# Optimization experiments

Measured on AMD Instinct MI355X. Metric: run time of the kernel, lower is better.

The kernel has to match this reference:

```python
import jax, jax.numpy as jnp
import numpy as np

B, L, D = 2, 1024, 1024
H = 16
NL = 2
DFF = 4 * D
EPS = 1e-5
W_SCALE = 0.02


def rmsnorm(x, w):
    # x * rsqrt(mean(x^2, -1) + eps) * w   (computed in fp32 as in the torch code)
    xf = x.astype(jnp.float32)
    n = xf * jax.lax.rsqrt(jnp.mean(xf * xf, axis=-1, keepdims=True) + EPS)
    return n.astype(x.dtype) * w


def setup_inputs() -> dict:
    key = jax.random.key(0)
    ks = jax.random.split(key, 10)
    x = jax.random.normal(ks[0], (B, L, D), dtype=jnp.float32)
    # torch nn.Linear weight layout: [out_features, in_features]; y = x @ W.T + b
    qw = jax.random.normal(ks[1], (NL, D, D), dtype=jnp.float32) * W_SCALE
    kw = jax.random.normal(ks[2], (NL, D, D), dtype=jnp.float32) * W_SCALE
    vw = jax.random.normal(ks[3], (NL, D, D), dtype=jnp.float32) * W_SCALE
    ow = jax.random.normal(ks[4], (NL, D, D), dtype=jnp.float32) * W_SCALE
    pn_w = jnp.ones((NL, D), dtype=jnp.float32)
    ln_w = jnp.ones((NL, D), dtype=jnp.float32)
    fc_w = jax.random.normal(ks[5], (NL, DFF, D), dtype=jnp.float32) * W_SCALE
    fc2_w = jax.random.normal(ks[6], (NL, D, DFF), dtype=jnp.float32) * W_SCALE
    fc2_b = jnp.zeros((NL, D), dtype=jnp.float32)
    return {"x": x, "qw": qw, "kw": kw, "vw": vw, "ow": ow,
            "pn_w": pn_w, "ln_w": ln_w, "fc_w": fc_w, "fc2_w": fc2_w, "fc2_b": fc2_b}


def reference(x, qw, kw, vw, ow, pn_w, ln_w, fc_w, fc2_w, fc2_b):
    d = D // H
    for i in range(NL):
        # --- LinearAttention block (dropout=0 -> identity) ---
        h = rmsnorm(x, pn_w[i])                                   # [B,L,D]
        Q = (h @ qw[i].T).reshape(B, L, H, d)
        K = (h @ kw[i].T).reshape(B, L, H, d)
        V = (h @ vw[i].T).reshape(B, L, H, d)
        # outer-product state per position, cumulated over L (causal linear attn)
        W = jnp.einsum('blhd,blhe->blhde', K, V)                  # [B,L,H,d,d]
        W = jnp.cumsum(W, axis=1)
        a = jnp.einsum('blhd,blhde->blhe', Q, W).reshape(B, L, D)
        x = x + a @ ow[i].T
        # --- MLP block ---
        m = rmsnorm(x, ln_w[i])
        f = jax.nn.gelu(m @ fc_w[i].T, approximate=False)         # torch nn.GELU default = exact
        x = x + f @ fc2_w[i].T + fc2_b[i]
    return x
```

## Files before the change

kernel.cpp:

```cpp
#include <hip/hip_runtime.h>

#define BB 2
#define LL 1024
#define DD 1024
#define HH 16
#define HD 64
#define DFFN 4096
#define MM (BB*LL)
#define QS 3072

using u16 = unsigned short;
typedef __bf16 bf16x8 __attribute__((ext_vector_type(8)));
typedef float f32x4 __attribute__((ext_vector_type(4)));

__device__ __forceinline__ float b2f(u16 u) {
  union { unsigned int i; float f; } v; v.i = ((unsigned int)u) << 16; return v.f;
}
__device__ __forceinline__ u16 f2b(float f) {
  union { float f; unsigned int i; } v; v.f = f;
  unsigned int x = v.i;
  return (u16)((x + 0x7fffu + ((x >> 16) & 1u)) >> 16);
}
__device__ __forceinline__ float gelu_exact(float x) {
  return 0.5f * x * (1.0f + erff(x * 0.70710678118654752f));
}
__device__ __forceinline__ void gl2lds16(const void* g, void* l) {
  __builtin_amdgcn_global_load_lds((const __attribute__((address_space(1))) void*)g,
                                   (__attribute__((address_space(3))) void*)l, 16, 0, 0);
}

template<int N>
__device__ __forceinline__ void s_wait_vm() {
  if constexpr (N == 0)       asm volatile("s_waitcnt vmcnt(0)" ::: "memory");
  else if constexpr (N == 3)  asm volatile("s_waitcnt vmcnt(3)" ::: "memory");
  else if constexpr (N == 6)  asm volatile("s_waitcnt vmcnt(6)" ::: "memory");
  __builtin_amdgcn_sched_barrier(0);
}

__device__ __forceinline__ void xcd_remap(int& bx, int& by, int& bz) {
  const int gx = gridDim.x, gy = gridDim.y;
  const int nb = gx * gy * gridDim.z;
  int b = blockIdx.x + gx * (blockIdx.y + gy * blockIdx.z);
  if ((nb & 127) == 0) {
    const int xcd = b & 7, seq = b >> 3;
    b = (((seq >> 4) << 3) + xcd) * 16 + (seq & 15);
  }
  bx = b % gx; const int rest = b / gx;
  by = rest % gy; bz = rest / gy;
}

__global__ __launch_bounds__(256) void castw_kernel(const float* __restrict__ in,
                                                    u16* __restrict__ out, int n8) {
  int i = blockIdx.x * 256 + threadIdx.x;
  if (i >= n8) return;
  const float4 a = reinterpret_cast<const float4*>(in)[2 * i];
  const float4 b = reinterpret_cast<const float4*>(in)[2 * i + 1];
  uint4 o;
  o.x = (unsigned)f2b(a.x) | ((unsigned)f2b(a.y) << 16);
  o.y = (unsigned)f2b(a.z) | ((unsigned)f2b(a.w) << 16);
  o.z = (unsigned)f2b(b.x) | ((unsigned)f2b(b.y) << 16);
  o.w = (unsigned)f2b(b.z) | ((unsigned)f2b(b.w) << 16);
  reinterpret_cast<uint4*>(out)[i] = o;
}
__global__ __launch_bounds__(256) void castw3_kernel(const float* __restrict__ s0,
                                                     const float* __restrict__ s1,
                                                     const float* __restrict__ s2,
                                                     u16* __restrict__ out, int n8) {
  int i = blockIdx.x * 256 + threadIdx.x;
  if (i >= n8) return;
  const float* in = (blockIdx.y == 0) ? s0 : (blockIdx.y == 1) ? s1 : s2;
  u16* dst = out + (size_t)blockIdx.y * n8 * 8;
  const float4 a = reinterpret_cast<const float4*>(in)[2 * i];
  const float4 b = reinterpret_cast<const float4*>(in)[2 * i + 1];
  uint4 o;
  o.x = (unsigned)f2b(a.x) | ((unsigned)f2b(a.y) << 16);
  o.y = (unsigned)f2b(a.z) | ((unsigned)f2b(a.w) << 16);
  o.z = (unsigned)f2b(b.x) | ((unsigned)f2b(b.y) << 16);
  o.w = (unsigned)f2b(b.z) | ((unsigned)f2b(b.w) << 16);
  reinterpret_cast<uint4*>(dst)[i] = o;
}

__global__ __launch_bounds__(256) void init_out_kernel(float* __restrict__ out,
                                                       const float* __restrict__ resid,
                                                       const float* __restrict__ bias) {
  const int i = blockIdx.x * 256 + threadIdx.x;
  float4 v = reinterpret_cast<const float4*>(resid)[i];
  if (bias != nullptr) {
    const float4 bv = *reinterpret_cast<const float4*>(bias + ((i * 4) & (DD - 1)));
    v.x += bv.x; v.y += bv.y; v.z += bv.z; v.w += bv.w;
  }
  reinterpret_cast<float4*>(out)[i] = v;
}

__global__ __launch_bounds__(256) void rmsnorm_kernel(const float* __restrict__ x,
                                                      const float* __restrict__ w,
                                                      u16* __restrict__ out) {
  const int row = blockIdx.x, t = threadIdx.x;
  const float4 v = reinterpret_cast<const float4*>(x + (size_t)row * DD)[t];
  float ss = v.x*v.x + v.y*v.y + v.z*v.z + v.w*v.w;
  #pragma unroll
  for (int o = 32; o > 0; o >>= 1) ss += __shfl_down(ss, o);
  __shared__ float red[4];
  if ((t & 63) == 0) red[t >> 6] = ss;
  __syncthreads();
  const float inv = rsqrtf((red[0] + red[1] + red[2] + red[3]) * (1.0f / DD) + 1e-5f);
  const float4 wv = reinterpret_cast<const float4*>(w)[t];
  ushort4 o;
  o.x = f2b(v.x * inv * wv.x);
  o.y = f2b(v.y * inv * wv.y);
  o.z = f2b(v.z * inv * wv.z);
  o.w = f2b(v.w * inv * wv.w);
  reinterpret_cast<ushort4*>(out + (size_t)row * DD)[t] = o;
}

template<int ROWS, int NT>
__device__ __forceinline__ void dma32(const u16* __restrict__ g, int r0, int K, int kt,
                                      int t, u16* lds) {
  #pragma unroll
  for (int i = 0; i < ROWS * 4 / NT; i++) {
    const int c = i * NT + t;
    const int row = (c & 7) | ((c >> 5) << 3);
    const int kc = (c >> 3) & 3;
    gl2lds16(g + (size_t)(r0 + row) * K + kt + kc * 8, &lds[c * 8]);
  }
}
__device__ __forceinline__ const bf16x8* lds_frag(const u16* base, int r, int fq) {
  const int p = (r & 7) | (fq << 3) | ((r >> 3) << 5);
  return reinterpret_cast<const bf16x8*>(&base[p * 8]);
}

#define MFMA_BF16 __builtin_amdgcn_mfma_f32_16x16x32_bf16

template<int BM, int BN>
__device__ __forceinline__ void gemm_pipe(const u16* __restrict__ A,
                                          const u16* __restrict__ Wb,
                                          int K, int k0, int nt, int m0, int n0,
                                          u16* As, u16* Bs, int t,
                                          int wm, int wn, int fr, int fq,
                                          f32x4 acc[4][4]) {
  constexpr int NT = (BM / 64) * (BN / 64) * 64;
  #pragma unroll
  for (int s = 0; s < 3; ++s) {
    dma32<BM, NT>(A, m0, K, k0 + s * 32, t, As + s * BM * 32);
    dma32<BN, NT>(Wb, n0, K, k0 + s * 32, t, Bs + s * BN * 32);
  }
  s_wait_vm<6>();
  __builtin_amdgcn_s_barrier();
  int pb = 0;
  for (int tt = 0; tt < nt; ++tt) {
    const u16* Asb = As + pb * BM * 32;
    const u16* Bsb = Bs + pb * BN * 32;
    const int p3 = (pb + 3) & 3;
    const bool st = (tt + 3 < nt);
    bf16x8 a0 = *lds_frag(Asb, wm + 0 * 16 + fr, fq);
    bf16x8 a1 = *lds_frag(Asb, wm + 1 * 16 + fr, fq);
    bf16x8 b0 = *lds_frag(Bsb, wn + 0 * 16 + fr, fq);
    bf16x8 b1 = *lds_frag(Bsb, wn + 1 * 16 + fr, fq);
    bf16x8 b2 = *lds_frag(Bsb, wn + 2 * 16 + fr, fq);
    bf16x8 b3 = *lds_frag(Bsb, wn + 3 * 16 + fr, fq);
    if (st) dma32<BM, NT>(A, m0, K, k0 + (tt + 3) * 32, t, As + p3 * BM * 32);
    __builtin_amdgcn_sched_barrier(0);
    __builtin_amdgcn_s_barrier();
    asm volatile("s_waitcnt lgkmcnt(0)" ::: "memory");
    __builtin_amdgcn_sched_barrier(0);
    __builtin_amdgcn_s_setprio(1);
    acc[0][0] = MFMA_BF16(a0, b0, acc[0][0], 0, 0, 0);
    acc[0][1] = MFMA_BF16(a0, b1, acc[0][1], 0, 0, 0);
    acc[0][2] = MFMA_BF16(a0, b2, acc[0][2], 0, 0, 0);
    acc[0][3] = MFMA_BF16(a0, b3, acc[0][3], 0, 0, 0);
    acc[1][0] = MFMA_BF16(a1, b0, acc[1][0], 0, 0, 0);
    acc[1][1] = MFMA_BF16(a1, b1, acc[1][1], 0, 0, 0);
    acc[1][2] = MFMA_BF16(a1, b2, acc[1][2], 0, 0, 0);
    acc[1][3] = MFMA_BF16(a1, b3, acc[1][3], 0, 0, 0);
    __builtin_amdgcn_s_setprio(0);
    __builtin_amdgcn_sched_barrier(0);
    __builtin_amdgcn_s_barrier();
    bf16x8 a2 = *lds_frag(Asb, wm + 2 * 16 + fr, fq);
    bf16x8 a3 = *lds_frag(Asb, wm + 3 * 16 + fr, fq);
    if (st) dma32<BN, NT>(Wb, n0, K, k0 + (tt + 3) * 32, t, Bs + p3 * BN * 32);
    __builtin_amdgcn_sched_barrier(0);
    __builtin_amdgcn_s_barrier();
    asm volatile("s_waitcnt lgkmcnt(0)" ::: "memory");
    __builtin_amdgcn_sched_barrier(0);
    __builtin_amdgcn_s_setprio(1);
    acc[2][0] = MFMA_BF16(a2, b0, acc[2][0], 0, 0, 0);
    acc[2][1] = MFMA_BF16(a2, b1, acc[2][1], 0, 0, 0);
    acc[2][2] = MFMA_BF16(a2, b2, acc[2][2], 0, 0, 0);
    acc[2][3] = MFMA_BF16(a2, b3, acc[2][3], 0, 0, 0);
    acc[3][0] = MFMA_BF16(a3, b0, acc[3][0], 0, 0, 0);
    acc[3][1] = MFMA_BF16(a3, b1, acc[3][1], 0, 0, 0);
    acc[3][2] = MFMA_BF16(a3, b2, acc[3][2], 0, 0, 0);
    acc[3][3] = MFMA_BF16(a3, b3, acc[3][3], 0, 0, 0);
    __builtin_amdgcn_s_setprio(0);
    __builtin_amdgcn_sched_barrier(0);
    if (tt + 1 < nt) {
      const int rem = nt - 2 - tt;
      if (rem >= 2)      s_wait_vm<6>();
      else if (rem == 1) s_wait_vm<3>();
      else               s_wait_vm<0>();
      __builtin_amdgcn_s_barrier();
    }
    pb = (pb + 1) & 3;
  }
}

template<int BM, int BN, int ACT>
__global__ __launch_bounds__((BM/64)*(BN/64)*64)
void mfma_gemm(const u16* __restrict__ A, const u16* __restrict__ Wb,
               u16* __restrict__ Cb, int N, int K) {
  constexpr int WCOLS = BN / 64;
  __shared__ u16 As[4 * BM * 32];
  __shared__ u16 Bs[4 * BN * 32];
  int bx, by, bz;
  xcd_remap(bx, by, bz);
  const int t = threadIdx.x;
  const int lane = t & 63, w = t >> 6;
  const int wm = (w / WCOLS) * 64, wn = (w % WCOLS) * 64;
  const int m0 = by * BM, n0 = bx * BN;
  const int fr = lane & 15, fq = lane >> 4;

  f32x4 acc[4][4] = {};
  gemm_pipe<BM, BN>(A, Wb, K, 0, K / 32, m0, n0, As, Bs, t, wm, wn, fr, fq, acc);

  #pragma unroll
  for (int i = 0; i < 4; i++)
    #pragma unroll
    for (int j = 0; j < 4; j++)
      #pragma unroll
      for (int r = 0; r < 4; r++) {
        const int row = m0 + wm + i * 16 + fq * 4 + r;
        const int col = n0 + wn + j * 16 + fr;
        float val = acc[i][j][r];
        if (ACT == 1) val = gelu_exact(val);
        Cb[(size_t)row * N + col] = f2b(val);
      }
}

template<int BM, int BN, int SPLIT>
__global__ __launch_bounds__((BM/64)*(BN/64)*64)
void mfma_gemm_sk(const u16* __restrict__ A, const u16* __restrict__ Wb,
                  float* __restrict__ Co, int N, int K) {
  constexpr int WCOLS = BN / 64;
  __shared__ u16 As[4 * BM * 32];
  __shared__ u16 Bs[4 * BN * 32];
  int bx, by, bz;
  xcd_remap(bx, by, bz);
  const int t = threadIdx.x;
  const int lane = t & 63, w = t >> 6;
  const int wm = (w / WCOLS) * 64, wn = (w % WCOLS) * 64;
  const int m0 = by * BM, n0 = bx * BN;
  const int fr = lane & 15, fq = lane >> 4;
  const int Kc = K / SPLIT, k0 = bz * Kc;

  f32x4 acc[4][4] = {};
  gemm_pipe<BM, BN>(A, Wb, K, k0, Kc / 32, m0, n0, As, Bs, t, wm, wn, fr, fq, acc);

  #pragma unroll
  for (int i = 0; i < 4; i++)
    #pragma unroll
    for (int j = 0; j < 4; j++)
      #pragma unroll
      for (int r = 0; r < 4; r++) {
        const int row = m0 + wm + i * 16 + fq * 4 + r;
        const int col = n0 + wn + j * 16 + fr;
        unsafeAtomicAdd(&Co[(size_t)row * N + col], acc[i][j][r]);
      }
}

__global__ __launch_bounds__(256) void kv_trans(const u16* __restrict__ QKV,
                                                u16* __restrict__ Kt, u16* __restrict__ Vt) {
  __shared__ u16 T[64][72];
  const int tile = blockIdx.x;
  const int h2 = blockIdx.y;
  const int b = blockIdx.z;
  const int h = h2 & 15, which = h2 >> 4;
  const int t = threadIdx.x;
  const int pos = t >> 2, d0 = (t & 3) * 16;
  const u16* src = QKV + ((size_t)(b * LL) + tile * 64 + pos) * QS + 1024 + which * 1024 + h * HD + d0;
  union { uint4 u[2]; u16 s[16]; } pk;
  pk.u[0] = reinterpret_cast<const uint4*>(src)[0];
  pk.u[1] = reinterpret_cast<const uint4*>(src)[1];
  #pragma unroll
  for (int j = 0; j < 16; j++) T[d0 + j][pos] = pk.s[j];
  __syncthreads();
  const int d = t >> 2, p0 = (t & 3) * 16;
  u16* dst = (which ? Vt : Kt) + ((size_t)(b * HH + h) * HD + d) * LL + tile * 64 + p0;
  union { uint4 u[2]; u16 s[16]; } ok;
  #pragma unroll
  for (int j = 0; j < 16; j++) ok.s[j] = T[d][p0 + j];
  reinterpret_cast<uint4*>(dst)[0] = ok.u[0];
  reinterpret_cast<uint4*>(dst)[1] = ok.u[1];
}

__global__ __launch_bounds__(256) void attn_phase1(const u16* __restrict__ QKV,
                                                   const u16* __restrict__ Kt,
                                                   const u16* __restrict__ Vt,
                                                   u16* __restrict__ Oa,
                                                   u16* __restrict__ Slt) {
  __shared__ u16 Ss[4][16][64];
  const int tile = blockIdx.x, h = blockIdx.y, b = blockIdx.z;
  const int t = threadIdx.x, lane = t & 63, w = t >> 6;
  const int fr = lane & 15, fq = lane >> 4;
  const size_t tok0 = (size_t)(b * LL + tile * 64);
  const size_t bh = (size_t)(b * HH + h);
  const u16* Qb  = QKV + tok0 * QS + h * HD;
  const u16* Kb  = Qb + 1024;
  const u16* Ktb = Kt + bh * (HD * LL) + tile * 64;
  const u16* Vtb = Vt + bh * (HD * LL) + tile * 64;

  bf16x8 aq[2], bk[4][2];
  #pragma unroll
  for (int kh = 0; kh < 2; kh++)
    aq[kh] = *reinterpret_cast<const bf16x8*>(Qb + (size_t)(16*w + fr) * QS + kh*32 + fq*8);
  #pragma unroll
  for (int n4 = 0; n4 < 4; n4++)
    #pragma unroll
    for (int kh = 0; kh < 2; kh++)
      bk[n4][kh] = *reinterpret_cast<const bf16x8*>(Kb + (size_t)(16*n4 + fr) * QS + kh*32 + fq*8);
  f32x4 sacc[4] = {};
  #pragma unroll
  for (int n4 = 0; n4 < 4; n4++) {
    sacc[n4] = MFMA_BF16(aq[0], bk[n4][0], sacc[n4], 0, 0, 0);
    sacc[n4] = MFMA_BF16(aq[1], bk[n4][1], sacc[n4], 0, 0, 0);
  }
  #pragma unroll
  for (int n4 = 0; n4 < 4; n4++)
    #pragma unroll
    for (int r = 0; r < 4; r++) {
      const bool keep = (16*w + 4*fq + r) >= (16*n4 + fr);
      Ss[w][4*fq + r][16*n4 + fr] = keep ? f2b(sacc[n4][r]) : (u16)0;
    }
  __syncthreads();

  bf16x8 va[2], kt[4][2];
  #pragma unroll
  for (int kh = 0; kh < 2; kh++)
    va[kh] = *reinterpret_cast<const bf16x8*>(Vtb + (size_t)(16*w + fr) * LL + kh*32 + fq*8);
  #pragma unroll
  for (int n4 = 0; n4 < 4; n4++)
    #pragma unroll
    for (int kh = 0; kh < 2; kh++)
      kt[n4][kh] = *reinterpret_cast<const bf16x8*>(Ktb + (size_t)(16*n4 + fr) * LL + kh*32 + fq*8);
  f32x4 lacc[4] = {};
  #pragma unroll
  for (int n4 = 0; n4 < 4; n4++) {
    lacc[n4] = MFMA_BF16(va[0], kt[n4][0], lacc[n4], 0, 0, 0);
    lacc[n4] = MFMA_BF16(va[1], kt[n4][1], lacc[n4], 0, 0, 0);
  }
  u16* So = Slt + (bh * 16 + tile) * 4096;
  #pragma unroll
  for (int n4 = 0; n4 < 4; n4++)
    #pragma unroll
    for (int r = 0; r < 4; r++)
      So[(size_t)(16*w + 4*fq + r) * 64 + 16*n4 + fr] = f2b(lacc[n4][r]);

  bf16x8 sa[2], vb[4][2];
  #pragma unroll
  for (int kh = 0; kh < 2; kh++)
    sa[kh] = *reinterpret_cast<const bf16x8*>(&Ss[w][fr][kh*32 + fq*8]);
  #pragma unroll
  for (int n4 = 0; n4 < 4; n4++)
    #pragma unroll
    for (int kh = 0; kh < 2; kh++)
      vb[n4][kh] = *reinterpret_cast<const bf16x8*>(Vtb + (size_t)(16*n4 + fr) * LL + kh*32 + fq*8);
  f32x4 oacc[4] = {};
  #pragma unroll
  for (int n4 = 0; n4 < 4; n4++) {
    oacc[n4] = MFMA_BF16(sa[0], vb[n4][0], oacc[n4], 0, 0, 0);
    oacc[n4] = MFMA_BF16(sa[1], vb[n4][1], oacc[n4], 0, 0, 0);
  }
  u16* Ob = Oa + (tok0 + 16*w) * DD + h * HD;
  #pragma unroll
  for (int n4 = 0; n4 < 4; n4++)
    #pragma unroll
    for (int r = 0; r < 4; r++)
      Ob[(size_t)(4*fq + r) * DD + 16*n4 + fr] = f2b(oacc[n4][r]);
}

__global__ __launch_bounds__(256) void attn_phase2(const u16* __restrict__ Slt,
                                                   u16* __restrict__ Wc) {
  const int rg = blockIdx.x, h = blockIdx.y, b = blockIdx.z;
  const size_t base = ((size_t)((b * HH + h) * 16)) * 4096 + rg * 512 + threadIdx.x * 2;
  float r0 = 0.f, r1 = 0.f;
  for (int tl = 0; tl < 16; tl++) {
    const size_t p = base + (size_t)tl * 4096;
    const unsigned d = *reinterpret_cast<const unsigned*>(Slt + p);
    *reinterpret_cast<unsigned*>(Wc + p) = (unsigned)f2b(r0) | ((unsigned)f2b(r1) << 16);
    r0 += b2f((u16)(d & 0xffff));
    r1 += b2f((u16)(d >> 16));
  }
}

__global__ __launch_bounds__(256) void attn_phase3(const u16* __restrict__ QKV,
                                                   const u16* __restrict__ Wc,
                                                   u16* __restrict__ Oa) {
  const int tile = blockIdx.x, h = blockIdx.y, b = blockIdx.z;
  const int t = threadIdx.x, lane = t & 63, w = t >> 6;
  const int fr = lane & 15, fq = lane >> 4;
  const size_t tok0 = (size_t)(b * LL + tile * 64);
  const size_t bh = (size_t)(b * HH + h);
  const u16* Qb = QKV + tok0 * QS + h * HD;
  const u16* Wb = Wc + (bh * 16 + tile) * 4096;

  bf16x8 aq[2], wb[4][2];
  #pragma unroll
  for (int kh = 0; kh < 2; kh++)
    aq[kh] = *reinterpret_cast<const bf16x8*>(Qb + (size_t)(16*w + fr) * QS + kh*32 + fq*8);
  #pragma unroll
  for (int n4 = 0; n4 < 4; n4++)
    #pragma unroll
    for (int kh = 0; kh < 2; kh++)
      wb[n4][kh] = *reinterpret_cast<const bf16x8*>(Wb + (size_t)(16*n4 + fr) * 64 + kh*32 + fq*8);
  f32x4 oacc[4] = {};
  #pragma unroll
  for (int n4 = 0; n4 < 4; n4++) {
    oacc[n4] = MFMA_BF16(aq[0], wb[n4][0], oacc[n4], 0, 0, 0);
    oacc[n4] = MFMA_BF16(aq[1], wb[n4][1], oacc[n4], 0, 0, 0);
  }
  u16* Ob = Oa + (tok0 + 16*w) * DD + h * HD;
  #pragma unroll
  for (int n4 = 0; n4 < 4; n4++)
    #pragma unroll
    for (int r = 0; r < 4; r++) {
      const size_t idx = (size_t)(4*fq + r) * DD + 16*n4 + fr;
      Ob[idx] = f2b(b2f(Ob[idx]) + oacc[n4][r]);
    }
}

extern "C" void kernel_launch(void* const* d_in, const int* in_sizes, int n_in,
                              void* d_out, int out_size, void* d_ws, size_t ws_size,
                              hipStream_t stream) {
  const float* x_in = (const float*)d_in[0];
  const float* qw   = (const float*)d_in[1];
  const float* kw   = (const float*)d_in[2];
  const float* vw   = (const float*)d_in[3];
  const float* ow   = (const float*)d_in[4];
  const float* pn   = (const float*)d_in[5];
  const float* ln   = (const float*)d_in[6];
  const float* fcw  = (const float*)d_in[7];
  const float* fc2w = (const float*)d_in[8];
  const float* fc2b = (const float*)d_in[9];

  char* ws = (char*)d_ws;
  u16* wbuf = (u16*)ws;
  u16* slt  = (u16*)ws;
  u16* wcum = (u16*)(ws + (size_t)(4 << 20));
  u16* h    = (u16*)(ws + (size_t)(8 << 20));
  u16* qkv  = (u16*)(ws + (size_t)(12 << 20));
  u16* f    = (u16*)(ws + (size_t)(12 << 20));
  u16* vt   = (u16*)(ws + (size_t)(24 << 20));
  u16* kt   = (u16*)(ws + (size_t)(28 << 20));
  float* xf = (float*)d_out;

  const int n8D = DD * DD / 8;
  const int n8F = DFFN * DD / 8;
  const int gInit = MM * DD / 4 / 256;

  for (int i = 0; i < 2; i++) {
    const float* qwi  = qw   + (size_t)i * DD * DD;
    const float* kwi  = kw   + (size_t)i * DD * DD;
    const float* vwi  = vw   + (size_t)i * DD * DD;
    const float* owi  = ow   + (size_t)i * DD * DD;
    const float* fcwi = fcw  + (size_t)i * DFFN * DD;
    const float* f2wi = fc2w + (size_t)i * DD * DFFN;
    const float* src  = (i == 0) ? x_in : xf;

    rmsnorm_kernel<<<MM, 256, 0, stream>>>(src, pn + i * DD, h);
    castw3_kernel<<<dim3(n8D / 256, 3), 256, 0, stream>>>(qwi, kwi, vwi, wbuf, n8D);
    mfma_gemm<256, 128, 0><<<dim3(QS / 128, MM / 256), 512, 0, stream>>>(
        h, wbuf, qkv, QS, DD);
    kv_trans<<<dim3(16, 32, BB), 256, 0, stream>>>(qkv, kt, vt);
    attn_phase1<<<dim3(16, HH, BB), 256, 0, stream>>>(qkv, kt, vt, h, slt);
    attn_phase2<<<dim3(8, HH, BB), 256, 0, stream>>>(slt, wcum);
    attn_phase3<<<dim3(16, HH, BB), 256, 0, stream>>>(qkv, wcum, h);
    castw_kernel<<<n8D / 256, 256, 0, stream>>>(owi, wbuf, n8D);
    init_out_kernel<<<gInit, 256, 0, stream>>>(xf, src, nullptr);
    mfma_gemm_sk<256, 128, 4><<<dim3(DD / 128, MM / 256, 4), 512, 0, stream>>>(
        h, wbuf, xf, DD, DD);
    rmsnorm_kernel<<<MM, 256, 0, stream>>>(xf, ln + i * DD, h);
    castw_kernel<<<n8F / 256, 256, 0, stream>>>(fcwi, wbuf, n8F);
    mfma_gemm<256, 128, 1><<<dim3(DFFN / 128, MM / 256), 512, 0, stream>>>(
        h, wbuf, f, DFFN, DD);
    castw_kernel<<<n8F / 256, 256, 0, stream>>>(f2wi, wbuf, n8F);
    float* co = (i == 1) ? (float*)d_out : xf;
    init_out_kernel<<<gInit, 256, 0, stream>>>(co, xf, fc2b + i * DD);
    mfma_gemm_sk<256, 128, 4><<<dim3(DD / 128, MM / 256, 4), 512, 0, stream>>>(
        f, wbuf, co, DD, DFFN);
  }
}
```

Measured before the change: 581.5 us.

## Replace atomic split-K output GEMMs with fused residual epilogue and partial buffers

Drops the init_out kernels and the atomic split-K accumulation. The O-projection now runs as a single-pass 128x64 tile GEMM whose epilogue adds the residual directly. FC2 uses a 2-way split where slice 0 writes residual+bias+acc and slice 1 writes fp32 partials, which a separate reduce kernel adds back. The pipeline wait counts are generalized for smaller tiles. This removes atomics and an extra full pass over the output, at the cost of smaller tiles with fewer threads, a partial buffer round-trip, and a new reduce launch.

```diff
diff --git a/kernel.cpp b/kernel.cpp
--- a/kernel.cpp
+++ b/kernel.cpp
@@ -34,6 +34,7 @@
   if constexpr (N == 0)       asm volatile("s_waitcnt vmcnt(0)" ::: "memory");
   else if constexpr (N == 3)  asm volatile("s_waitcnt vmcnt(3)" ::: "memory");
   else if constexpr (N == 6)  asm volatile("s_waitcnt vmcnt(6)" ::: "memory");
+  else if constexpr (N == 12) asm volatile("s_waitcnt vmcnt(12)" ::: "memory");
   __builtin_amdgcn_sched_barrier(0);
 }
 
@@ -80,18 +81,6 @@
   reinterpret_cast<uint4*>(dst)[i] = o;
 }
 
-__global__ __launch_bounds__(256) void init_out_kernel(float* __restrict__ out,
-                                                       const float* __restrict__ resid,
-                                                       const float* __restrict__ bias) {
-  const int i = blockIdx.x * 256 + threadIdx.x;
-  float4 v = reinterpret_cast<const float4*>(resid)[i];
-  if (bias != nullptr) {
-    const float4 bv = *reinterpret_cast<const float4*>(bias + ((i * 4) & (DD - 1)));
-    v.x += bv.x; v.y += bv.y; v.z += bv.z; v.w += bv.w;
-  }
-  reinterpret_cast<float4*>(out)[i] = v;
-}
-
 __global__ __launch_bounds__(256) void rmsnorm_kernel(const float* __restrict__ x,
                                                       const float* __restrict__ w,
                                                       u16* __restrict__ out) {
@@ -113,6 +102,18 @@
   reinterpret_cast<ushort4*>(out + (size_t)row * DD)[t] = o;
 }
 
+__global__ __launch_bounds__(256) void reduce_add_kernel(float* __restrict__ co,
+                                                         const float* __restrict__ P0,
+                                                         const float* __restrict__ P1) {
+  const int i = blockIdx.x * 256 + threadIdx.x;
+  constexpr int HALF = (MM / 2) * DD / 4;
+  const float4 p = (i < HALF) ? reinterpret_cast<const float4*>(P0)[i]
+                              : reinterpret_cast<const float4*>(P1)[i - HALF];
+  float4 v = reinterpret_cast<float4*>(co)[i];
+  v.x += p.x; v.y += p.y; v.z += p.z; v.w += p.w;
+  reinterpret_cast<float4*>(co)[i] = v;
+}
+
 template<int ROWS, int NT>
 __device__ __forceinline__ void dma32(const u16* __restrict__ g, int r0, int K, int kt,
                                       int t, u16* lds) {
@@ -139,12 +140,13 @@
                                           int wm, int wn, int fr, int fq,
                                           f32x4 acc[4][4]) {
   constexpr int NT = (BM / 64) * (BN / 64) * 64;
+  constexpr int LT = (BM + BN) * 4 / NT;
   #pragma unroll
   for (int s = 0; s < 3; ++s) {
     dma32<BM, NT>(A, m0, K, k0 + s * 32, t, As + s * BM * 32);
     dma32<BN, NT>(Wb, n0, K, k0 + s * 32, t, Bs + s * BN * 32);
   }
-  s_wait_vm<6>();
+  s_wait_vm<2 * LT>();
   __builtin_amdgcn_s_barrier();
   int pb = 0;
   for (int tt = 0; tt < nt; ++tt) {
@@ -195,8 +197,8 @@
     __builtin_amdgcn_sched_barrier(0);
     if (tt + 1 < nt) {
       const int rem = nt - 2 - tt;
-      if (rem >= 2)      s_wait_vm<6>();
-      else if (rem == 1) s_wait_vm<3>();
+      if (rem >= 2)      s_wait_vm<2 * LT>();
+      else if (rem == 1) s_wait_vm<LT>();
       else               s_wait_vm<0>();
       __builtin_amdgcn_s_barrier();
     }
@@ -236,10 +238,12 @@
       }
 }
 
-template<int BM, int BN, int SPLIT>
+template<int BM, int BN>
 __global__ __launch_bounds__((BM/64)*(BN/64)*64)
-void mfma_gemm_sk(const u16* __restrict__ A, const u16* __restrict__ Wb,
-                  float* __restrict__ Co, int N, int K) {
+void mfma_gemm_fo(const u16* __restrict__ A, const u16* __restrict__ Wb,
+                  const float* __restrict__ resid, const float* __restrict__ bias,
+                  float* __restrict__ Co, float* __restrict__ P0, float* __restrict__ P1,
+                  int N, int K, int Kc) {
   constexpr int WCOLS = BN / 64;
   __shared__ u16 As[4 * BM * 32];
   __shared__ u16 Bs[4 * BN * 32];
@@ -250,21 +254,39 @@
   const int wm = (w / WCOLS) * 64, wn = (w % WCOLS) * 64;
   const int m0 = by * BM, n0 = bx * BN;
   const int fr = lane & 15, fq = lane >> 4;
-  const int Kc = K / SPLIT, k0 = bz * Kc;
+  const int k0 = bz * Kc;
 
   f32x4 acc[4][4] = {};
   gemm_pipe<BM, BN>(A, Wb, K, k0, Kc / 32, m0, n0, As, Bs, t, wm, wn, fr, fq, acc);
 
-  #pragma unroll
-  for (int i = 0; i < 4; i++)
-    #pragma unroll
-    for (int j = 0; j < 4; j++)
+  if (bz == 0) {
+    #pragma unroll
+    for (int j = 0; j < 4; j++) {
+      const int col = n0 + wn + j * 16 + fr;
+      const float bj = (bias != nullptr) ? bias[col] : 0.0f;
       #pragma unroll
-      for (int r = 0; r < 4; r++) {
-        const int row = m0 + wm + i * 16 + fq * 4 + r;
-        const int col = n0 + wn + j * 16 + fr;
-        unsafeAtomicAdd(&Co[(size_t)row * N + col], acc[i][j][r]);
-      }
+      for (int i = 0; i < 4; i++)
+        #pragma unroll
+        for (int r = 0; r < 4; r++) {
+          const int row = m0 + wm + i * 16 + fq * 4 + r;
+          const size_t idx = (size_t)row * N + col;
+          Co[idx] = resid[idx] + bj + acc[i][j][r];
+        }
+    }
+  } else {
+    #pragma unroll
+    for (int j = 0; j < 4; j++) {
+      const int col = n0 + wn + j * 16 + fr;
+      #pragma unroll
+      for (int i = 0; i < 4; i++)
+        #pragma unroll
+        for (int r = 0; r < 4; r++) {
+          const int row = m0 + wm + i * 16 + fq * 4 + r;
+          float* P = (row < MM / 2) ? P0 : P1;
+          P[(size_t)(row & (MM / 2 - 1)) * N + col] = acc[i][j][r];
+        }
+    }
+  }
 }
 
 __global__ __launch_bounds__(256) void kv_trans(const u16* __restrict__ QKV,
@@ -450,11 +472,12 @@
   u16* f    = (u16*)(ws + (size_t)(12 << 20));
   u16* vt   = (u16*)(ws + (size_t)(24 << 20));
   u16* kt   = (u16*)(ws + (size_t)(28 << 20));
+  float* p0 = (float*)(ws + (size_t)(8 << 20));
+  float* p1 = (float*)(ws + (size_t)(28 << 20));
   float* xf = (float*)d_out;
 
   const int n8D = DD * DD / 8;
   const int n8F = DFFN * DD / 8;
-  const int gInit = MM * DD / 4 / 256;
 
   for (int i = 0; i < 2; i++) {
     const float* qwi  = qw   + (size_t)i * DD * DD;
@@ -474,17 +497,16 @@
     attn_phase2<<<dim3(8, HH, BB), 256, 0, stream>>>(slt, wcum);
     attn_phase3<<<dim3(16, HH, BB), 256, 0, stream>>>(qkv, wcum, h);
     castw_kernel<<<n8D / 256, 256, 0, stream>>>(owi, wbuf, n8D);
-    init_out_kernel<<<gInit, 256, 0, stream>>>(xf, src, nullptr);
-    mfma_gemm_sk<256, 128, 4><<<dim3(DD / 128, MM / 256, 4), 512, 0, stream>>>(
-        h, wbuf, xf, DD, DD);
+    mfma_gemm_fo<128, 64><<<dim3(DD / 64, MM / 128, 1), 128, 0, stream>>>(
+        h, wbuf, src, nullptr, xf, p0, p1, DD, DD, DD);
     rmsnorm_kernel<<<MM, 256, 0, stream>>>(xf, ln + i * DD, h);
     castw_kernel<<<n8F / 256, 256, 0, stream>>>(fcwi, wbuf, n8F);
     mfma_gemm<256, 128, 1><<<dim3(DFFN / 128, MM / 256), 512, 0, stream>>>(
         h, wbuf, f, DFFN, DD);
     castw_kernel<<<n8F / 256, 256, 0, stream>>>(f2wi, wbuf, n8F);
     float* co = (i == 1) ? (float*)d_out : xf;
-    init_out_kernel<<<gInit, 256, 0, stream>>>(co, xf, fc2b + i * DD);
-    mfma_gemm_sk<256, 128, 4><<<dim3(DD / 128, MM / 256, 4), 512, 0, stream>>>(
-        f, wbuf, co, DD, DFFN);
-  }
-}
+    mfma_gemm_fo<128, 64><<<dim3(DD / 64, MM / 128, 2), 128, 0, stream>>>(
+        f, wbuf, xf, fc2b + i * DD, co, p0, p1, DD, DFFN, DFFN / 2);
+    reduce_add_kernel<<<MM * DD / 4 / 256, 256, 0, stream>>>(co, p0, p1);
+  }
+}
```

Result: no change. 571.1 us (-1.8%).
